# Kernel tuning notes

Hardware: AMD Instinct MI355X
Metric: run time of the kernel (lower is better)

Reference implementation:

```python
import jax, jax.numpy as jnp
import numpy as np

BLOCK_SIZES = [256] * 8            # sum = N_CTX = 2048
B, H, D = 2, 16, 64
N_CTX = sum(BLOCK_SIZES)
SPARSITY_PATTERN = 'block_causal'  # row_starts = 0, row_ends = end of own block


def _build_masks(block_sizes, pattern):
    cs = np.cumsum([0] + list(block_sizes))
    row_ends = np.concatenate([np.full(bs, cs[i + 1], dtype=np.int32)
                               for i, bs in enumerate(block_sizes)])
    if pattern == 'block_diagonal':
        row_starts = np.concatenate([np.full(bs, cs[i], dtype=np.int32)
                                     for i, bs in enumerate(block_sizes)])
    elif pattern == 'block_causal':
        row_starts = np.zeros_like(row_ends)
    else:
        raise ValueError(pattern)
    return jnp.asarray(row_starts), jnp.asarray(row_ends)


def setup_inputs() -> dict:
    key = jax.random.key(0)
    kq, kk, kv = jax.random.split(key, 3)
    q = jax.random.normal(kq, (B, H, N_CTX, D), dtype=jnp.float32)
    k = jax.random.normal(kk, (B, H, N_CTX, D), dtype=jnp.float32)
    v = jax.random.normal(kv, (B, H, N_CTX, D), dtype=jnp.float32)
    row_starts, row_ends = _build_masks(BLOCK_SIZES, SPARSITY_PATTERN)
    sm_scale = jnp.float32(1.0 / np.sqrt(D))
    return {"q": q, "k": k, "v": v, "sm_scale": sm_scale,
            "row_starts": row_starts, "row_ends": row_ends}


def reference(q, k, v, sm_scale, row_starts, row_ends):
    # q,k,v: [B,H,N,D]; per query row i, attend to kv cols in [row_starts[i], row_ends[i])
    n = q.shape[2]
    cols = jnp.arange(n, dtype=jnp.int32)
    allowed = (cols[None, :] >= row_starts[:, None]) & (cols[None, :] < row_ends[:, None])  # [N,N]
    scores = jnp.einsum('bhqd,bhkd->bhqk', q, k) * sm_scale
    neg = jnp.finfo(scores.dtype).min
    scores = jnp.where(allowed[None, None], scores, neg)
    p = jax.nn.softmax(scores, axis=-1)
    return jnp.einsum('bhqk,bhkd->bhqd', p, v)
```

## Files before the change

kernel.cpp:

```cpp
#include <hip/hip_runtime.h>


typedef short bf16x8 __attribute__((ext_vector_type(8)));
typedef short bf16x4 __attribute__((ext_vector_type(4)));
typedef float f32x4  __attribute__((ext_vector_type(4)));

#define MFMA(A, B, C) __builtin_amdgcn_mfma_f32_16x16x32_bf16((A), (B), (C), 0, 0, 0)

__device__ __forceinline__ short f2bf(float f) {
    union { float f; unsigned u; } c; c.f = f;
    unsigned r = c.u + 0x7FFFu + ((c.u >> 16) & 1u);
    return (short)(r >> 16);
}

__global__ __launch_bounds__(512, 4)
void bsattn_kernel(const float* __restrict__ Q, const float* __restrict__ K,
                   const float* __restrict__ V, const float* __restrict__ SC,
                   const int* __restrict__ RS, const int* __restrict__ RE,
                   float* __restrict__ O)
{
    constexpr int N = 2048, D = 64, LSTR = 72;

    int wg   = blockIdx.x;
    int slot = wg >> 8;
    int r    = wg & 255;
    int i8   = r >> 5;
    int bh   = r & 31;
    int qt   = (slot == 0) ? (15 - i8) : i8;
    int q0   = qt << 7;

    int tid  = threadIdx.x;
    int wid  = tid >> 6;
    int lane = tid & 63;
    int n    = lane & 15;
    int g    = lane >> 4;

    const size_t bho = (size_t)bh * (N * D);
    const float* Qb = Q + bho;
    const float* Kb = K + bho;
    const float* Vb = V + bho;
    float*       Ob = O + bho;

    __shared__ __align__(16) short lk[64 * LSTR];
    __shared__ __align__(16) short lv[64 * LSTR];
    __shared__ int sb[2][4];

    if (tid < 128) {
        int rs = RS[q0 + tid];
        int re = RE[q0 + tid];
        int a = rs, b = rs, c = re, d = re;
        #pragma unroll
        for (int off = 32; off > 0; off >>= 1) {
            a = min(a, __shfl_xor(a, off));
            b = max(b, __shfl_xor(b, off));
            c = min(c, __shfl_xor(c, off));
            d = max(d, __shfl_xor(d, off));
        }
        if (lane == 0) { sb[wid][0] = a; sb[wid][1] = b; sb[wid][2] = c; sb[wid][3] = d; }
    }

    int myrow = q0 + wid * 16 + n;
    int rs_l  = RS[myrow];
    int re_l  = RE[myrow];

    float sscale = SC[0] * 1.44269504088896340736f;

    bf16x8 qf0, qf1;
    {
        const float* qp = Qb + (size_t)myrow * D + g * 8;
        float4 a0 = *(const float4*)(qp);
        float4 a1 = *(const float4*)(qp + 4);
        float4 b0 = *(const float4*)(qp + 32);
        float4 b1 = *(const float4*)(qp + 36);
        qf0[0] = f2bf(a0.x * sscale); qf0[1] = f2bf(a0.y * sscale);
        qf0[2] = f2bf(a0.z * sscale); qf0[3] = f2bf(a0.w * sscale);
        qf0[4] = f2bf(a1.x * sscale); qf0[5] = f2bf(a1.y * sscale);
        qf0[6] = f2bf(a1.z * sscale); qf0[7] = f2bf(a1.w * sscale);
        qf1[0] = f2bf(b0.x * sscale); qf1[1] = f2bf(b0.y * sscale);
        qf1[2] = f2bf(b0.z * sscale); qf1[3] = f2bf(b0.w * sscale);
        qf1[4] = f2bf(b1.x * sscale); qf1[5] = f2bf(b1.y * sscale);
        qf1[6] = f2bf(b1.z * sscale); qf1[7] = f2bf(b1.w * sscale);
    }

    __syncthreads();
    int rs_min = min(sb[0][0], sb[1][0]);
    int rs_max = max(sb[0][1], sb[1][1]);
    int re_min = min(sb[0][2], sb[1][2]);
    int re_max = max(sb[0][3], sb[1][3]);

    f32x4 acc0 = {0.f, 0.f, 0.f, 0.f};
    f32x4 acc1 = acc0, acc2 = acc0, acc3 = acc0;
    float m_run = -1e30f, l_run = 0.f;

    for (int kt = (rs_min & ~63); kt < re_max; kt += 64) {
        __syncthreads();
        #pragma unroll
        for (int it = 0; it < 2; ++it) {
            int f   = it * 512 + tid;
            int key = f >> 4;
            int d0  = (f & 15) << 2;
            float4 kv = *(const float4*)(Kb + (size_t)(kt + key) * D + d0);
            bf16x4 kp;
            kp[0] = f2bf(kv.x); kp[1] = f2bf(kv.y); kp[2] = f2bf(kv.z); kp[3] = f2bf(kv.w);
            *(bf16x4*)(&lk[key * LSTR + d0]) = kp;
            float4 vv = *(const float4*)(Vb + (size_t)(kt + key) * D + d0);
            lv[(d0 + 0) * LSTR + key] = f2bf(vv.x);
            lv[(d0 + 1) * LSTR + key] = f2bf(vv.y);
            lv[(d0 + 2) * LSTR + key] = f2bf(vv.z);
            lv[(d0 + 3) * LSTR + key] = f2bf(vv.w);
        }
        __syncthreads();

        #pragma unroll
        for (int half = 0; half < 2; ++half) {
            int kb0 = kt + half * 32;
            int row0 = half * 32 + ((n >> 2) << 3) + (n & 3);
            const bf16x8* a00 = (const bf16x8*)&lk[row0 * LSTR + g * 8];
            const bf16x8* a01 = (const bf16x8*)&lk[row0 * LSTR + 32 + g * 8];
            const bf16x8* a10 = (const bf16x8*)&lk[(row0 + 4) * LSTR + g * 8];
            const bf16x8* a11 = (const bf16x8*)&lk[(row0 + 4) * LSTR + 32 + g * 8];
            f32x4 s0 = {0.f, 0.f, 0.f, 0.f};
            f32x4 s1 = {0.f, 0.f, 0.f, 0.f};
            s0 = MFMA(*a00, qf0, s0);
            s0 = MFMA(*a01, qf1, s0);
            s1 = MFMA(*a10, qf0, s1);
            s1 = MFMA(*a11, qf1, s1);

            float sc8[8] = { s0[0], s0[1], s0[2], s0[3], s1[0], s1[1], s1[2], s1[3] };
            if (kb0 < rs_max || kb0 + 32 > re_min) {
                #pragma unroll
                for (int j = 0; j < 8; ++j) {
                    int key = kb0 + g * 8 + j;
                    if (key < rs_l || key >= re_l) sc8[j] = -1e30f;
                }
            }
            float tmax = sc8[0];
            #pragma unroll
            for (int j = 1; j < 8; ++j) tmax = fmaxf(tmax, sc8[j]);
            tmax = fmaxf(tmax, __shfl_xor(tmax, 16));
            tmax = fmaxf(tmax, __shfl_xor(tmax, 32));
            float m_new = fmaxf(m_run, tmax);
            float alpha = __builtin_amdgcn_exp2f(m_run - m_new);
            float psum = 0.f;
            bf16x8 pf;
            #pragma unroll
            for (int j = 0; j < 8; ++j) {
                float p = (sc8[j] > -0.5e30f) ? __builtin_amdgcn_exp2f(sc8[j] - m_new) : 0.f;
                psum += p;
                pf[j] = f2bf(p);
            }
            psum += __shfl_xor(psum, 16);
            psum += __shfl_xor(psum, 32);
            l_run = l_run * alpha + psum;
            m_run = m_new;

            int rbase = g << 2;
            float al0 = __shfl(alpha, rbase + 0);
            float al1 = __shfl(alpha, rbase + 1);
            float al2 = __shfl(alpha, rbase + 2);
            float al3 = __shfl(alpha, rbase + 3);
            acc0[0] *= al0; acc0[1] *= al1; acc0[2] *= al2; acc0[3] *= al3;
            acc1[0] *= al0; acc1[1] *= al1; acc1[2] *= al2; acc1[3] *= al3;
            acc2[0] *= al0; acc2[1] *= al1; acc2[2] *= al2; acc2[3] *= al3;
            acc3[0] *= al0; acc3[1] *= al1; acc3[2] *= al2; acc3[3] *= al3;

            int klocal = half * 32 + g * 8;
            const bf16x8* v0 = (const bf16x8*)&lv[(0  + n) * LSTR + klocal];
            const bf16x8* v1 = (const bf16x8*)&lv[(16 + n) * LSTR + klocal];
            const bf16x8* v2 = (const bf16x8*)&lv[(32 + n) * LSTR + klocal];
            const bf16x8* v3 = (const bf16x8*)&lv[(48 + n) * LSTR + klocal];
            acc0 = MFMA(pf, *v0, acc0);
            acc1 = MFMA(pf, *v1, acc1);
            acc2 = MFMA(pf, *v2, acc2);
            acc3 = MFMA(pf, *v3, acc3);
        }
    }

    float linv = 1.0f / l_run;
    int rbase = g << 2;
    float li[4];
    li[0] = __shfl(linv, rbase + 0);
    li[1] = __shfl(linv, rbase + 1);
    li[2] = __shfl(linv, rbase + 2);
    li[3] = __shfl(linv, rbase + 3);
    int orow = q0 + wid * 16 + rbase;
    #pragma unroll
    for (int reg = 0; reg < 4; ++reg) {
        float* rp = Ob + (size_t)(orow + reg) * D + n;
        rp[0]  = acc0[reg] * li[reg];
        rp[16] = acc1[reg] * li[reg];
        rp[32] = acc2[reg] * li[reg];
        rp[48] = acc3[reg] * li[reg];
    }
}

extern "C" void kernel_launch(void* const* d_in, const int* in_sizes, int n_in,
                              void* d_out, int out_size, void* d_ws, size_t ws_size,
                              hipStream_t stream) {
    const float* q  = (const float*)d_in[0];
    const float* k  = (const float*)d_in[1];
    const float* v  = (const float*)d_in[2];
    const float* sc = (const float*)d_in[3];
    const int* rs   = (const int*)d_in[4];
    const int* re   = (const int*)d_in[5];
    float* out      = (float*)d_out;
    bsattn_kernel<<<dim3(512), dim3(512), 0, stream>>>(q, k, v, sc, rs, re, out);
}
```

Baseline: 155.5 us.

## Pre-convert K/V to swizzled bf16 blob and drop online softmax max tracking

Adds a prep kernel that converts K and V once into a bf16 workspace blob. K is stored in a rotated, swizzled layout and V is pre-transposed, so the attention kernel copies tiles straight into LDS instead of re-converting fp32 K/V in every workgroup. The main kernel now uses 64-row query tiles with 256 threads and processes 128 keys per sync. It removes the running max and rescaling of online softmax and computes the row sum with an MFMA against a ones vector. Skipping the max subtraction risks overflow or precision loss when score magnitudes are large, and it adds an extra kernel launch plus a workspace round trip.

```diff
diff --git a/kernel.cpp b/kernel.cpp
--- a/kernel.cpp
+++ b/kernel.cpp
@@ -2,195 +2,200 @@
 
 
 typedef short bf16x8 __attribute__((ext_vector_type(8)));
-typedef short bf16x4 __attribute__((ext_vector_type(4)));
 typedef float f32x4  __attribute__((ext_vector_type(4)));
-
-#define MFMA(A, B, C) __builtin_amdgcn_mfma_f32_16x16x32_bf16((A), (B), (C), 0, 0, 0)
-
-__device__ __forceinline__ short f2bf(float f) {
+typedef unsigned short u16;
+typedef u16 u16x8 __attribute__((ext_vector_type(8)));
+
+#define MFMA(A,B,C) __builtin_amdgcn_mfma_f32_16x16x32_bf16((A),(B),(C),0,0,0)
+
+__device__ __forceinline__ u16 f2bf_rne(float f) {
     union { float f; unsigned u; } c; c.f = f;
     unsigned r = c.u + 0x7FFFu + ((c.u >> 16) & 1u);
-    return (short)(r >> 16);
-}
-
-__global__ __launch_bounds__(512, 4)
-void bsattn_kernel(const float* __restrict__ Q, const float* __restrict__ K,
-                   const float* __restrict__ V, const float* __restrict__ SC,
-                   const int* __restrict__ RS, const int* __restrict__ RE,
-                   float* __restrict__ O)
+    return (u16)(r >> 16);
+}
+__device__ __forceinline__ u16 f2bf_fast(float f) {
+    union { float f; unsigned u; } c; c.f = f;
+    return (u16)((c.u + 0x8000u) >> 16);
+}
+
+__global__ __launch_bounds__(256)
+void prep_kernel(const float* __restrict__ K, const float* __restrict__ V,
+                 u16* __restrict__ blob)
 {
-    constexpr int N = 2048, D = 64, LSTR = 72;
-
-    int wg   = blockIdx.x;
-    int slot = wg >> 8;
-    int r    = wg & 255;
-    int i8   = r >> 5;
-    int bh   = r & 31;
-    int qt   = (slot == 0) ? (15 - i8) : i8;
-    int q0   = qt << 7;
-
-    int tid  = threadIdx.x;
-    int wid  = tid >> 6;
-    int lane = tid & 63;
-    int n    = lane & 15;
-    int g    = lane >> 4;
-
-    const size_t bho = (size_t)bh * (N * D);
-    const float* Qb = Q + bho;
-    const float* Kb = K + bho;
-    const float* Vb = V + bho;
-    float*       Ob = O + bho;
-
-    __shared__ __align__(16) short lk[64 * LSTR];
-    __shared__ __align__(16) short lv[64 * LSTR];
-    __shared__ int sb[2][4];
-
-    if (tid < 128) {
-        int rs = RS[q0 + tid];
-        int re = RE[q0 + tid];
-        int a = rs, b = rs, c = re, d = re;
-        #pragma unroll
-        for (int off = 32; off > 0; off >>= 1) {
-            a = min(a, __shfl_xor(a, off));
-            b = max(b, __shfl_xor(b, off));
-            c = min(c, __shfl_xor(c, off));
-            d = max(d, __shfl_xor(d, off));
-        }
-        if (lane == 0) { sb[wid][0] = a; sb[wid][1] = b; sb[wid][2] = c; sb[wid][3] = d; }
-    }
+    int bt = blockIdx.x;
+    int tid = threadIdx.x;
+    const size_t gbase = (size_t)bt * 4096;
+    u16* bb = blob + (size_t)bt * 8192;
+    __shared__ __align__(16) u16 lt[4096];
+
+    int key = tid >> 2;
+    int c2  = (tid & 3) << 1;
+    int rotb = (key & 3) + 4 * ((key >> 3) & 1);
+    {
+        const float* kp = K + gbase + key * 64 + c2 * 8;
+        float4 x0 = *(const float4*)kp,       x1 = *(const float4*)(kp + 4);
+        float4 x2 = *(const float4*)(kp + 8), x3 = *(const float4*)(kp + 12);
+        u16x8 a, b;
+        a[0]=f2bf_rne(x0.x); a[1]=f2bf_rne(x0.y); a[2]=f2bf_rne(x0.z); a[3]=f2bf_rne(x0.w);
+        a[4]=f2bf_rne(x1.x); a[5]=f2bf_rne(x1.y); a[6]=f2bf_rne(x1.z); a[7]=f2bf_rne(x1.w);
+        b[0]=f2bf_rne(x2.x); b[1]=f2bf_rne(x2.y); b[2]=f2bf_rne(x2.z); b[3]=f2bf_rne(x2.w);
+        b[4]=f2bf_rne(x3.x); b[5]=f2bf_rne(x3.y); b[6]=f2bf_rne(x3.z); b[7]=f2bf_rne(x3.w);
+        *(u16x8*)&bb[key * 64 + (((c2    ) + rotb) & 7) * 8] = a;
+        *(u16x8*)&bb[key * 64 + (((c2 + 1) + rotb) & 7) * 8] = b;
+    }
+    {
+        const float* vp = V + gbase + key * 64 + c2 * 8;
+        float4 y0 = *(const float4*)vp,       y1 = *(const float4*)(vp + 4);
+        float4 y2 = *(const float4*)(vp + 8), y3 = *(const float4*)(vp + 12);
+        float yy[16] = { y0.x,y0.y,y0.z,y0.w, y1.x,y1.y,y1.z,y1.w,
+                         y2.x,y2.y,y2.z,y2.w, y3.x,y3.y,y3.z,y3.w };
+        int kc = key >> 3, kw = key & 7;
+        #pragma unroll
+        for (int j = 0; j < 16; ++j) {
+            int d = c2 * 8 + j;
+            lt[d * 64 + ((kc + (d & 7)) & 7) * 8 + kw] = f2bf_rne(yy[j]);
+        }
+    }
+    __syncthreads();
+    {
+        int o = tid * 16;
+        *(u16x8*)&bb[4096 + o]     = *(const u16x8*)&lt[o];
+        *(u16x8*)&bb[4096 + o + 8] = *(const u16x8*)&lt[o + 8];
+    }
+}
+
+__global__ __launch_bounds__(256, 4)
+void bsattn_main(const float* __restrict__ Q, const float* __restrict__ SC,
+                 const int* __restrict__ RS, const int* __restrict__ RE,
+                 const u16* __restrict__ blob, float* __restrict__ O)
+{
+    constexpr int N = 2048, D = 64;
+    int wg = blockIdx.x;
+    int bh = wg & 31, qt = wg >> 5;
+    int q0 = qt << 6;
+    int tid = threadIdx.x, wid = tid >> 6, lane = tid & 63;
+    int n = lane & 15, g = lane >> 4;
+
+    __shared__ __align__(16) u16 lsm[16384];
+    __shared__ int sb[4][2];
 
     int myrow = q0 + wid * 16 + n;
-    int rs_l  = RS[myrow];
-    int re_l  = RE[myrow];
+    int rs_l = RS[myrow], re_l = RE[myrow];
+    int w_rs_min = rs_l, w_rs_max = rs_l, w_re_min = re_l, w_re_max = re_l;
+    #pragma unroll
+    for (int o = 1; o < 16; o <<= 1) {
+        w_rs_min = min(w_rs_min, __shfl_xor(w_rs_min, o));
+        w_rs_max = max(w_rs_max, __shfl_xor(w_rs_max, o));
+        w_re_min = min(w_re_min, __shfl_xor(w_re_min, o));
+        w_re_max = max(w_re_max, __shfl_xor(w_re_max, o));
+    }
+    if (lane == 0) { sb[wid][0] = w_rs_min; sb[wid][1] = w_re_max; }
 
     float sscale = SC[0] * 1.44269504088896340736f;
 
     bf16x8 qf0, qf1;
     {
-        const float* qp = Qb + (size_t)myrow * D + g * 8;
-        float4 a0 = *(const float4*)(qp);
-        float4 a1 = *(const float4*)(qp + 4);
-        float4 b0 = *(const float4*)(qp + 32);
-        float4 b1 = *(const float4*)(qp + 36);
-        qf0[0] = f2bf(a0.x * sscale); qf0[1] = f2bf(a0.y * sscale);
-        qf0[2] = f2bf(a0.z * sscale); qf0[3] = f2bf(a0.w * sscale);
-        qf0[4] = f2bf(a1.x * sscale); qf0[5] = f2bf(a1.y * sscale);
-        qf0[6] = f2bf(a1.z * sscale); qf0[7] = f2bf(a1.w * sscale);
-        qf1[0] = f2bf(b0.x * sscale); qf1[1] = f2bf(b0.y * sscale);
-        qf1[2] = f2bf(b0.z * sscale); qf1[3] = f2bf(b0.w * sscale);
-        qf1[4] = f2bf(b1.x * sscale); qf1[5] = f2bf(b1.y * sscale);
-        qf1[6] = f2bf(b1.z * sscale); qf1[7] = f2bf(b1.w * sscale);
+        const float* qp = Q + ((size_t)bh * N + myrow) * D + g * 8;
+        float4 a0 = *(const float4*)qp,        a1 = *(const float4*)(qp + 4);
+        float4 b0 = *(const float4*)(qp + 32), b1 = *(const float4*)(qp + 36);
+        qf0[0]=f2bf_rne(a0.x*sscale); qf0[1]=f2bf_rne(a0.y*sscale);
+        qf0[2]=f2bf_rne(a0.z*sscale); qf0[3]=f2bf_rne(a0.w*sscale);
+        qf0[4]=f2bf_rne(a1.x*sscale); qf0[5]=f2bf_rne(a1.y*sscale);
+        qf0[6]=f2bf_rne(a1.z*sscale); qf0[7]=f2bf_rne(a1.w*sscale);
+        qf1[0]=f2bf_rne(b0.x*sscale); qf1[1]=f2bf_rne(b0.y*sscale);
+        qf1[2]=f2bf_rne(b0.z*sscale); qf1[3]=f2bf_rne(b0.w*sscale);
+        qf1[4]=f2bf_rne(b1.x*sscale); qf1[5]=f2bf_rne(b1.y*sscale);
+        qf1[6]=f2bf_rne(b1.z*sscale); qf1[7]=f2bf_rne(b1.w*sscale);
     }
 
     __syncthreads();
-    int rs_min = min(sb[0][0], sb[1][0]);
-    int rs_max = max(sb[0][1], sb[1][1]);
-    int re_min = min(sb[0][2], sb[1][2]);
-    int re_max = max(sb[0][3], sb[1][3]);
-
-    f32x4 acc0 = {0.f, 0.f, 0.f, 0.f};
-    f32x4 acc1 = acc0, acc2 = acc0, acc3 = acc0;
-    float m_run = -1e30f, l_run = 0.f;
-
-    for (int kt = (rs_min & ~63); kt < re_max; kt += 64) {
-        __syncthreads();
-        #pragma unroll
-        for (int it = 0; it < 2; ++it) {
-            int f   = it * 512 + tid;
-            int key = f >> 4;
-            int d0  = (f & 15) << 2;
-            float4 kv = *(const float4*)(Kb + (size_t)(kt + key) * D + d0);
-            bf16x4 kp;
-            kp[0] = f2bf(kv.x); kp[1] = f2bf(kv.y); kp[2] = f2bf(kv.z); kp[3] = f2bf(kv.w);
-            *(bf16x4*)(&lk[key * LSTR + d0]) = kp;
-            float4 vv = *(const float4*)(Vb + (size_t)(kt + key) * D + d0);
-            lv[(d0 + 0) * LSTR + key] = f2bf(vv.x);
-            lv[(d0 + 1) * LSTR + key] = f2bf(vv.y);
-            lv[(d0 + 2) * LSTR + key] = f2bf(vv.z);
-            lv[(d0 + 3) * LSTR + key] = f2bf(vv.w);
-        }
-        __syncthreads();
-
-        #pragma unroll
-        for (int half = 0; half < 2; ++half) {
-            int kb0 = kt + half * 32;
-            int row0 = half * 32 + ((n >> 2) << 3) + (n & 3);
-            const bf16x8* a00 = (const bf16x8*)&lk[row0 * LSTR + g * 8];
-            const bf16x8* a01 = (const bf16x8*)&lk[row0 * LSTR + 32 + g * 8];
-            const bf16x8* a10 = (const bf16x8*)&lk[(row0 + 4) * LSTR + g * 8];
-            const bf16x8* a11 = (const bf16x8*)&lk[(row0 + 4) * LSTR + 32 + g * 8];
-            f32x4 s0 = {0.f, 0.f, 0.f, 0.f};
-            f32x4 s1 = {0.f, 0.f, 0.f, 0.f};
-            s0 = MFMA(*a00, qf0, s0);
-            s0 = MFMA(*a01, qf1, s0);
-            s1 = MFMA(*a10, qf0, s1);
-            s1 = MFMA(*a11, qf1, s1);
-
-            float sc8[8] = { s0[0], s0[1], s0[2], s0[3], s1[0], s1[1], s1[2], s1[3] };
-            if (kb0 < rs_max || kb0 + 32 > re_min) {
+    int kst  = min(min(sb[0][0], sb[1][0]), min(sb[2][0], sb[3][0])) & ~63;
+    int kend = max(max(sb[0][1], sb[1][1]), max(sb[2][1], sb[3][1]));
+
+    int rA  = ((n >> 2) << 3) + (n & 3);
+    int phk = (n & 3) + 4 * ((n >> 2) & 1);
+    int osA0 = rA * 64 + ((g     + phk) & 7) * 8;
+    int osA1 = rA * 64 + ((g + 4 + phk) & 7) * 8;
+    int ov0 = 4096 + n * 64 + ((    g + (n & 7)) & 7) * 8;
+    int ov1 = 4096 + n * 64 + ((4 + g + (n & 7)) & 7) * 8;
+
+    f32x4 acc[4], accl = {0.f, 0.f, 0.f, 0.f};
+    #pragma unroll
+    for (int c = 0; c < 4; ++c) acc[c] = (f32x4){0.f, 0.f, 0.f, 0.f};
+    bf16x8 ones;
+    #pragma unroll
+    for (int j = 0; j < 8; ++j) ones[j] = (short)0x3F80;
+
+    auto proc = [&](int kb, const u16* ls) {
+        float sc[16];
+        #pragma unroll
+        for (int h = 0; h < 2; ++h) {
+            int hb = h * 2048;
+            f32x4 t0 = {0.f,0.f,0.f,0.f}, t1 = t0;
+            t0 = MFMA(*(const bf16x8*)&ls[hb + osA0],       qf0, t0);
+            t0 = MFMA(*(const bf16x8*)&ls[hb + osA1],       qf1, t0);
+            t1 = MFMA(*(const bf16x8*)&ls[hb + osA0 + 256], qf0, t1);
+            t1 = MFMA(*(const bf16x8*)&ls[hb + osA1 + 256], qf1, t1);
+            #pragma unroll
+            for (int r = 0; r < 4; ++r) { sc[h*8 + r] = t0[r]; sc[h*8 + 4 + r] = t1[r]; }
+        }
+        if (kb < w_rs_max || kb + 64 > w_re_min) {
+            #pragma unroll
+            for (int h = 0; h < 2; ++h)
                 #pragma unroll
                 for (int j = 0; j < 8; ++j) {
-                    int key = kb0 + g * 8 + j;
-                    if (key < rs_l || key >= re_l) sc8[j] = -1e30f;
+                    int key = kb + h * 32 + g * 8 + j;
+                    if (key < rs_l || key >= re_l) sc[h*8 + j] = -1e30f;
                 }
+        }
+        bf16x8 pf0, pf1;
+        #pragma unroll
+        for (int j = 0; j < 8; ++j) { float p = __builtin_amdgcn_exp2f(sc[j]);     pf0[j] = (short)f2bf_fast(p); }
+        #pragma unroll
+        for (int j = 0; j < 8; ++j) { float p = __builtin_amdgcn_exp2f(sc[8 + j]); pf1[j] = (short)f2bf_fast(p); }
+        #pragma unroll
+        for (int h = 0; h < 2; ++h) {
+            const bf16x8& pf = h ? pf1 : pf0;
+            int ov = h ? ov1 : ov0;
+            acc[0] = MFMA(pf, *(const bf16x8*)&ls[ov       ], acc[0]);
+            acc[1] = MFMA(pf, *(const bf16x8*)&ls[ov + 1024], acc[1]);
+            acc[2] = MFMA(pf, *(const bf16x8*)&ls[ov + 2048], acc[2]);
+            acc[3] = MFMA(pf, *(const bf16x8*)&ls[ov + 3072], acc[3]);
+            accl   = MFMA(pf, ones, accl);
+        }
+    };
+
+    for (int kt = kst; kt < kend; kt += 128) {
+        __syncthreads();
+        bool two = (kt + 64) < kend;
+        const u16* src = blob + ((size_t)(bh * 32) + (kt >> 6)) * 8192;
+        int cnt = two ? 4 : 2;
+        #pragma unroll
+        for (int i = 0; i < 4; ++i) {
+            if (i < cnt) {
+                int o = i * 4096 + tid * 16;
+                *(u16x8*)&lsm[o]     = *(const u16x8*)&src[o];
+                *(u16x8*)&lsm[o + 8] = *(const u16x8*)&src[o + 8];
             }
-            float tmax = sc8[0];
-            #pragma unroll
-            for (int j = 1; j < 8; ++j) tmax = fmaxf(tmax, sc8[j]);
-            tmax = fmaxf(tmax, __shfl_xor(tmax, 16));
-            tmax = fmaxf(tmax, __shfl_xor(tmax, 32));
-            float m_new = fmaxf(m_run, tmax);
-            float alpha = __builtin_amdgcn_exp2f(m_run - m_new);
-            float psum = 0.f;
-            bf16x8 pf;
-            #pragma unroll
-            for (int j = 0; j < 8; ++j) {
-                float p = (sc8[j] > -0.5e30f) ? __builtin_amdgcn_exp2f(sc8[j] - m_new) : 0.f;
-                psum += p;
-                pf[j] = f2bf(p);
-            }
-            psum += __shfl_xor(psum, 16);
-            psum += __shfl_xor(psum, 32);
-            l_run = l_run * alpha + psum;
-            m_run = m_new;
-
-            int rbase = g << 2;
-            float al0 = __shfl(alpha, rbase + 0);
-            float al1 = __shfl(alpha, rbase + 1);
-            float al2 = __shfl(alpha, rbase + 2);
-            float al3 = __shfl(alpha, rbase + 3);
-            acc0[0] *= al0; acc0[1] *= al1; acc0[2] *= al2; acc0[3] *= al3;
-            acc1[0] *= al0; acc1[1] *= al1; acc1[2] *= al2; acc1[3] *= al3;
-            acc2[0] *= al0; acc2[1] *= al1; acc2[2] *= al2; acc2[3] *= al3;
-            acc3[0] *= al0; acc3[1] *= al1; acc3[2] *= al2; acc3[3] *= al3;
-
-            int klocal = half * 32 + g * 8;
-            const bf16x8* v0 = (const bf16x8*)&lv[(0  + n) * LSTR + klocal];
-            const bf16x8* v1 = (const bf16x8*)&lv[(16 + n) * LSTR + klocal];
-            const bf16x8* v2 = (const bf16x8*)&lv[(32 + n) * LSTR + klocal];
-            const bf16x8* v3 = (const bf16x8*)&lv[(48 + n) * LSTR + klocal];
-            acc0 = MFMA(pf, *v0, acc0);
-            acc1 = MFMA(pf, *v1, acc1);
-            acc2 = MFMA(pf, *v2, acc2);
-            acc3 = MFMA(pf, *v3, acc3);
-        }
-    }
-
-    float linv = 1.0f / l_run;
-    int rbase = g << 2;
-    float li[4];
-    li[0] = __shfl(linv, rbase + 0);
-    li[1] = __shfl(linv, rbase + 1);
-    li[2] = __shfl(linv, rbase + 2);
-    li[3] = __shfl(linv, rbase + 3);
-    int orow = q0 + wid * 16 + rbase;
-    #pragma unroll
-    for (int reg = 0; reg < 4; ++reg) {
-        float* rp = Ob + (size_t)(orow + reg) * D + n;
-        rp[0]  = acc0[reg] * li[reg];
-        rp[16] = acc1[reg] * li[reg];
-        rp[32] = acc2[reg] * li[reg];
-        rp[48] = acc3[reg] * li[reg];
+        }
+        __syncthreads();
+        if (kt < w_re_max && kt + 64 > w_rs_min)
+            proc(kt, lsm);
+        if (two && (kt + 64) < w_re_max && kt + 128 > w_rs_min)
+            proc(kt + 64, lsm + 8192);
+    }
+
+    int rb = g << 2;
+    int orow = q0 + wid * 16 + rb;
+    float* ob = O + ((size_t)bh * N + orow) * D + n;
+    #pragma unroll
+    for (int r = 0; r < 4; ++r) {
+        float li = 1.0f / accl[r];
+        float* rp = ob + (size_t)r * D;
+        rp[0]  = acc[0][r] * li;
+        rp[16] = acc[1][r] * li;
+        rp[32] = acc[2][r] * li;
+        rp[48] = acc[3][r] * li;
     }
 }
 
@@ -204,5 +209,8 @@
     const int* rs   = (const int*)d_in[4];
     const int* re   = (const int*)d_in[5];
     float* out      = (float*)d_out;
-    bsattn_kernel<<<dim3(512), dim3(512), 0, stream>>>(q, k, v, sc, rs, re, out);
-}
+    u16* blob       = (u16*)d_ws;
+
+    prep_kernel<<<dim3(1024), dim3(256), 0, stream>>>(k, v, blob);
+    bsattn_main<<<dim3(1024), dim3(256), 0, stream>>>(q, sc, rs, re, blob, out);
+}
```

New measurement: 135.4 us. 13.0% less time.
